# Performance work log

Measured on AMD Instinct MI355X. Metric: run time of the kernel, lower is better.

## Reference

```python
import jax, jax.numpy as jnp
import numpy as np

N_ITEMS = 100000
EMBED_DIM = 64
N_REL = 3
N_EDGES = 3200000


def setup_inputs() -> dict:
    key = jax.random.key(0)
    k1, k2, k3, k4 = jax.random.split(key, 4)
    item_embeddings = jax.random.normal(k1, (N_ITEMS, EMBED_DIM), dtype=jnp.float32)
    rows = jax.random.randint(k2, (N_REL, N_EDGES), 0, N_ITEMS, dtype=jnp.int64)
    cols = jax.random.randint(k3, (N_REL, N_EDGES), 0, N_ITEMS, dtype=jnp.int64)
    vals = jax.random.uniform(k4, (N_REL, N_EDGES), dtype=jnp.float32)
    return {"item_embeddings": item_embeddings, "rows": rows, "cols": cols, "vals": vals}


def reference(item_embeddings, rows, cols, vals):
    # item_embeddings: [N, D]; rows/cols/vals: [R, E] COO edge lists per relation.
    n_items, _ = item_embeddings.shape
    n_rel = rows.shape[0]
    rel_emb = jnp.zeros_like(item_embeddings)
    for r in range(n_rel):  # fixed small number of relation types
        # SpMM: neighbor_emb[i] = sum_{e: rows[e]==i} vals[e] * E[cols[e]]
        msgs = item_embeddings[cols[r]] * vals[r][:, None]          # [E, D]
        neighbor = jax.ops.segment_sum(msgs, rows[r], num_segments=n_items)  # [N, D]
        # degree = row sum of adjacency values, clamped to min 1
        degree = jax.ops.segment_sum(vals[r], rows[r], num_segments=n_items)  # [N]
        degree = jnp.maximum(degree, 1.0)
        rel_emb = rel_emb + neighbor / degree[:, None]
    rel_emb = rel_emb / n_rel
    return item_embeddings + rel_emb
```

## Files before the change

### kernel.cpp

```cpp
#include <hip/hip_runtime.h>

#define N_ITEMS     100000
#define EMBED_DIM   64
#define N_REL       3
#define N_EDGES     3200000
#define TOTAL_EDGES (N_REL * N_EDGES)
#define NKEY        (N_REL * N_ITEMS)

#define LOG_CH   6
#define CH_ROWS  64
#define NCHUNK   1563
#define NBKT     (NCHUNK * N_REL)
#define BCAP     2368
#define LOG_CB   12
#define NCB      25
#define TILEP    2048
#define NTILEP   ((N_EDGES + TILEP - 1) / TILEP)
#define SEGSB    68
#define CBCAP    (SEGSB * TILEP)

__global__ void initall_kernel(unsigned* __restrict__ gcursorF,
                               unsigned* __restrict__ cursorC) {
    int i = blockIdx.x * 256 + threadIdx.x;
    if (i < NBKT) gcursorF[i] = (unsigned)i * (unsigned)BCAP;
    if (i < N_REL * NCB) cursorC[i] = (unsigned)(i % NCB) * (unsigned)CBCAP;
}

__global__ void tobf16_kernel(const float* __restrict__ E, unsigned short* __restrict__ Ebf) {
    int i = blockIdx.x * 256 + threadIdx.x;
    if (i < N_ITEMS * EMBED_DIM) {
        unsigned u = __float_as_uint(E[i]);
        unsigned r = (u + 0x7FFFu + ((u >> 16) & 1u)) >> 16;
        Ebf[i] = (unsigned short)r;
    }
}

__launch_bounds__(512)
__global__ void partA2_kernel(const int* __restrict__ rows,
                              const int* __restrict__ cols,
                              const float* __restrict__ vals,
                              unsigned* __restrict__ cursorC,
                              uint2* __restrict__ coarse,
                              int rel0, unsigned relStrideU2) {
    __shared__ uint2 stag[TILEP];
    __shared__ unsigned char bkt[TILEP];
    __shared__ unsigned hist[NCB], lstart[NCB], gbase[NCB], lcur[NCB];
    int rel = rel0 + blockIdx.x / NTILEP;
    int base = (blockIdx.x % NTILEP) * TILEP;
    int cnt = N_EDGES - base; if (cnt > TILEP) cnt = TILEP;
    int t = threadIdx.x;
    const int go = rel * N_EDGES + base;
    uint2* __restrict__ coarseRel = coarse + (size_t)(rel - rel0) * relStrideU2;

    unsigned rrow[4], rcol[4], rval[4];
    #pragma unroll
    for (int k = 0; k < 4; k++) {
        int i = t + (k << 9);
        if (i < cnt) {
            rrow[k] = (unsigned)rows[go + i];
            rcol[k] = (unsigned)cols[go + i];
            rval[k] = __float_as_uint(vals[go + i]);
        } else rrow[k] = 0xFFFFFFFFu;
    }
    if (t < NCB) hist[t] = 0u;
    __syncthreads();
    #pragma unroll
    for (int k = 0; k < 4; k++)
        if (rrow[k] != 0xFFFFFFFFu) atomicAdd(&hist[rrow[k] >> LOG_CB], 1u);
    __syncthreads();
    if (t < 32) {
        unsigned v = (t < NCB) ? hist[t] : 0u;
        unsigned inc = v;
        #pragma unroll
        for (int d = 1; d < 32; d <<= 1) {
            unsigned x = __shfl_up(inc, d, 32);
            if (t >= d) inc += x;
        }
        if (t < NCB) {
            unsigned ex = inc - v;
            lstart[t] = ex; lcur[t] = ex;
            if (v) gbase[t] = atomicAdd(&cursorC[rel * NCB + t], v);
        }
    }
    __syncthreads();
    #pragma unroll
    for (int k = 0; k < 4; k++)
        if (rrow[k] != 0xFFFFFFFFu) {
            unsigned row = rrow[k];
            unsigned cb = row >> LOG_CB;
            unsigned dst = atomicAdd(&lcur[cb], 1u);
            stag[dst] = make_uint2(rcol[k] | ((row & 4095u) << 17), rval[k]);
            bkt[dst] = (unsigned char)cb;
        }
    __syncthreads();
    for (int i = t; i < cnt; i += 512) {
        unsigned bb = bkt[i];
        unsigned dst = gbase[bb] + ((unsigned)i - lstart[bb]);
        if (dst < (bb + 1u) * (unsigned)CBCAP) coarseRel[dst] = stag[i];
    }
}

__launch_bounds__(512)
__global__ void partB2_kernel(const unsigned* __restrict__ cursorC,
                              const uint2* __restrict__ coarse,
                              unsigned* __restrict__ gcursorF,
                              uint2* __restrict__ recs,
                              int rel0, unsigned relStrideU2) {
    __shared__ uint2 stag[TILEP];
    __shared__ unsigned char bkt[TILEP];
    __shared__ unsigned hist[64], lstart[64], gbase[64], lcur[64];
    int rel = rel0 + blockIdx.x / (NCB * SEGSB);
    int rem = blockIdx.x % (NCB * SEGSB);
    int cb = rem / SEGSB, seg = rem % SEGSB;
    unsigned cntA = cursorC[rel * NCB + cb] - (unsigned)cb * (unsigned)CBCAP;
    if (cntA > (unsigned)CBCAP) cntA = (unsigned)CBCAP;
    int off = seg * TILEP;
    int cnt = (int)cntA - off;
    if (cnt <= 0) return;
    if (cnt > TILEP) cnt = TILEP;
    const uint2* __restrict__ src = coarse + (size_t)(rel - rel0) * relStrideU2
                                  + (unsigned)cb * (unsigned)CBCAP + off;
    int t = threadIdx.x;

    uint2 rc[4];
    #pragma unroll
    for (int k = 0; k < 4; k++) {
        int i = t + (k << 9);
        rc[k] = (i < cnt) ? src[i] : make_uint2(0xFFFFFFFFu, 0u);
    }
    if (t < 64) hist[t] = 0u;
    __syncthreads();
    #pragma unroll
    for (int k = 0; k < 4; k++)
        if (rc[k].x != 0xFFFFFFFFu) atomicAdd(&hist[(rc[k].x >> 23) & 63u], 1u);
    __syncthreads();
    if (t < 64) {
        unsigned v = hist[t];
        unsigned inc = v;
        #pragma unroll
        for (int d = 1; d < 64; d <<= 1) {
            unsigned x = __shfl_up(inc, d, 64);
            if (t >= d) inc += x;
        }
        unsigned ex = inc - v;
        lstart[t] = ex; lcur[t] = ex;
        if (v) gbase[t] = atomicAdd(&gcursorF[(((unsigned)cb << 6) + t) * 3u + rel], v);
    }
    __syncthreads();
    #pragma unroll
    for (int k = 0; k < 4; k++)
        if (rc[k].x != 0xFFFFFFFFu) {
            unsigned j = (rc[k].x >> 23) & 63u;
            unsigned dst = atomicAdd(&lcur[j], 1u);
            stag[dst] = make_uint2(rc[k].x & 0x7FFFFFu, rc[k].y);
            bkt[dst] = (unsigned char)j;
        }
    __syncthreads();
    for (int i = t; i < cnt; i += 512) {
        unsigned j = bkt[i];
        unsigned bf = (((unsigned)cb << 6) + j) * 3u + rel;
        unsigned dst = gbase[j] + ((unsigned)i - lstart[j]);
        if (dst < (bf + 1u) * (unsigned)BCAP) recs[dst] = stag[i];
    }
}

__launch_bounds__(512, 8)
__global__ void gather_sort_kernel(const uint2* __restrict__ Ebf4,
                                   const float* __restrict__ E,
                                   const unsigned* __restrict__ gcursorF,
                                   const uint2* __restrict__ recs,
                                   float* __restrict__ out) {
    __shared__ uint2  srt[BCAP];
    __shared__ float4 accT4[CH_ROWS * 16];
    __shared__ unsigned hist[CH_ROWS], cur[CH_ROWS], rstart[CH_ROWS + 1];
    int c = blockIdx.x;
    int t = threadIdx.x;
    int w = t >> 6;
    int lane = t & 63;
    int sub = lane >> 4;
    int q = lane & 15;

    float* accT = (float*)accT4;
    for (int k = t; k < CH_ROWS * EMBED_DIM; k += 512) accT[k] = 0.f;

    for (int rel = 0; rel < N_REL; rel++) {
        unsigned b = (unsigned)(c * N_REL + rel);
        unsigned s0 = b * (unsigned)BCAP;
        int n = (int)(gcursorF[b] - s0);
        if (n > BCAP) n = BCAP;
        const uint2* __restrict__ pg = recs + s0;

        uint2 rc[5];
        #pragma unroll
        for (int k = 0; k < 5; k++) {
            int i = t + (k << 9);
            rc[k] = (i < n) ? pg[i] : make_uint2(0u, 0u);
        }
        if (t < CH_ROWS) hist[t] = 0u;
        __syncthreads();
        #pragma unroll
        for (int k = 0; k < 5; k++) {
            int i = t + (k << 9);
            if (i < n) atomicAdd(&hist[rc[k].x >> 17], 1u);
        }
        __syncthreads();
        if (t < 64) {
            unsigned v = hist[t];
            unsigned inc = v;
            #pragma unroll
            for (int d = 1; d < 64; d <<= 1) {
                unsigned x = __shfl_up(inc, d, 64);
                if (lane >= d) inc += x;
            }
            rstart[t] = inc - v;
            cur[t] = inc - v;
            if (t == 63) rstart[64] = inc;
        }
        __syncthreads();
        #pragma unroll
        for (int k = 0; k < 5; k++) {
            int i = t + (k << 9);
            if (i < n) {
                unsigned pos = atomicAdd(&cur[rc[k].x >> 17], 1u);
                srt[pos] = make_uint2(rc[k].x & 0x1FFFFu, rc[k].y);
            }
        }
        __syncthreads();

        for (int k = 0; k < 8; k++) {
            int r = (w << 3) + k;
            int base = (int)rstart[r];
            int nr = (int)(rstart[r + 1] - rstart[r]);
            float a0 = 0.f, a1 = 0.f, a2 = 0.f, a3 = 0.f, dg = 0.f;
            int i = sub;
            for (; i + 12 < nr; i += 16) {
                uint2 r0 = srt[base + i],     r1 = srt[base + i + 4];
                uint2 r2 = srt[base + i + 8], r3 = srt[base + i + 12];
                uint2 e0 = Ebf4[r0.x * 16u + q];
                uint2 e1 = Ebf4[r1.x * 16u + q];
                uint2 e2 = Ebf4[r2.x * 16u + q];
                uint2 e3 = Ebf4[r3.x * 16u + q];
                float w0 = __uint_as_float(r0.y), w1 = __uint_as_float(r1.y);
                float w2 = __uint_as_float(r2.y), w3 = __uint_as_float(r3.y);
                a0 += w0 * __uint_as_float(e0.x << 16);
                a1 += w0 * __uint_as_float(e0.x & 0xFFFF0000u);
                a2 += w0 * __uint_as_float(e0.y << 16);
                a3 += w0 * __uint_as_float(e0.y & 0xFFFF0000u);
                dg += w0;
                a0 += w1 * __uint_as_float(e1.x << 16);
                a1 += w1 * __uint_as_float(e1.x & 0xFFFF0000u);
                a2 += w1 * __uint_as_float(e1.y << 16);
                a3 += w1 * __uint_as_float(e1.y & 0xFFFF0000u);
                dg += w1;
                a0 += w2 * __uint_as_float(e2.x << 16);
                a1 += w2 * __uint_as_float(e2.x & 0xFFFF0000u);
                a2 += w2 * __uint_as_float(e2.y << 16);
                a3 += w2 * __uint_as_float(e2.y & 0xFFFF0000u);
                dg += w2;
                a0 += w3 * __uint_as_float(e3.x << 16);
                a1 += w3 * __uint_as_float(e3.x & 0xFFFF0000u);
                a2 += w3 * __uint_as_float(e3.y << 16);
                a3 += w3 * __uint_as_float(e3.y & 0xFFFF0000u);
                dg += w3;
            }
            for (; i < nr; i += 4) {
                uint2 r0 = srt[base + i];
                uint2 e0 = Ebf4[r0.x * 16u + q];
                float w0 = __uint_as_float(r0.y);
                a0 += w0 * __uint_as_float(e0.x << 16);
                a1 += w0 * __uint_as_float(e0.x & 0xFFFF0000u);
                a2 += w0 * __uint_as_float(e0.y << 16);
                a3 += w0 * __uint_as_float(e0.y & 0xFFFF0000u);
                dg += w0;
            }
            a0 += __shfl_xor(a0, 16, 64);  a0 += __shfl_xor(a0, 32, 64);
            a1 += __shfl_xor(a1, 16, 64);  a1 += __shfl_xor(a1, 32, 64);
            a2 += __shfl_xor(a2, 16, 64);  a2 += __shfl_xor(a2, 32, 64);
            a3 += __shfl_xor(a3, 16, 64);  a3 += __shfl_xor(a3, 32, 64);
            dg += __shfl_xor(dg, 16, 64);  dg += __shfl_xor(dg, 32, 64);
            float inv = 1.0f / (3.0f * fmaxf(dg, 1.0f));
            if (sub == 0) {
                float4 o = accT4[(r << 4) + q];
                accT4[(r << 4) + q] = make_float4(o.x + a0 * inv, o.y + a1 * inv,
                                                  o.z + a2 * inv, o.w + a3 * inv);
            }
        }
        __syncthreads();
    }

    int gbase2 = c * (CH_ROWS * EMBED_DIM);
    for (int k = t; k < CH_ROWS * EMBED_DIM; k += 512) {
        int gi = gbase2 + k;
        if (gi < N_ITEMS * EMBED_DIM) out[gi] = E[gi] + accT[k];
    }
}

#define NBS ((NKEY + 255) / 256)

__global__ void hist300_kernel(const int* __restrict__ rows, unsigned* __restrict__ cnt) {
    int stride = gridDim.x * blockDim.x;
    for (int i = blockIdx.x * blockDim.x + threadIdx.x; i < TOTAL_EDGES; i += stride) {
        unsigned r = (unsigned)i / (unsigned)N_EDGES;
        unsigned key = r * N_ITEMS + (unsigned)rows[i];
        atomicAdd(&cnt[key], 1u);
    }
}

__global__ void scan_blocksum(const unsigned* __restrict__ cnt, unsigned* __restrict__ bsum) {
    __shared__ unsigned s[256];
    int i = blockIdx.x * 256 + threadIdx.x;
    s[threadIdx.x] = (i < NKEY) ? cnt[i] : 0u;
    __syncthreads();
    for (int off = 128; off > 0; off >>= 1) {
        if (threadIdx.x < off) s[threadIdx.x] += s[threadIdx.x + off];
        __syncthreads();
    }
    if (threadIdx.x == 0) bsum[blockIdx.x] = s[0];
}

__global__ void scan_partials(unsigned* __restrict__ bsum, unsigned* __restrict__ starts) {
    const int IT = 5;
    int t = threadIdx.x;
    unsigned loc[IT];
    unsigned sum = 0;
    #pragma unroll
    for (int k = 0; k < IT; k++) {
        int idx = t * IT + k;
        loc[k] = (idx < NBS) ? bsum[idx] : 0u;
        sum += loc[k];
    }
    int lane = t & 63, wid = t >> 6;
    unsigned inc = sum;
    #pragma unroll
    for (int d = 1; d < 64; d <<= 1) {
        unsigned x = __shfl_up(inc, d, 64);
        if (lane >= d) inc += x;
    }
    __shared__ unsigned woff[4], woffEx[4];
    if (lane == 63) woff[wid] = inc;
    __syncthreads();
    if (t == 0) { unsigned run = 0; for (int k = 0; k < 4; k++) { woffEx[k] = run; run += woff[k]; } }
    __syncthreads();
    unsigned ex = inc - sum + woffEx[wid];
    #pragma unroll
    for (int k = 0; k < IT; k++) {
        int idx = t * IT + k;
        if (idx < NBS) { bsum[idx] = ex; ex += loc[k]; }
    }
    if (t == 0) starts[NKEY] = (unsigned)TOTAL_EDGES;
}

__global__ void scan_final(unsigned* key_arr,
                           const unsigned* __restrict__ bsum,
                           unsigned* __restrict__ cursor) {
    int i = blockIdx.x * 256 + threadIdx.x;
    unsigned v = (i < NKEY) ? key_arr[i] : 0u;
    int lane = threadIdx.x & 63, wid = threadIdx.x >> 6;
    unsigned inc = v;
    #pragma unroll
    for (int d = 1; d < 64; d <<= 1) {
        unsigned x = __shfl_up(inc, d, 64);
        if (lane >= d) inc += x;
    }
    __shared__ unsigned woff[4], woffEx[4];
    if (lane == 63) woff[wid] = inc;
    __syncthreads();
    if (threadIdx.x == 0) { unsigned run = 0; for (int k = 0; k < 4; k++) { woffEx[k] = run; run += woff[k]; } }
    __syncthreads();
    unsigned ex = inc - v + woffEx[wid] + bsum[blockIdx.x];
    if (i < NKEY) { key_arr[i] = ex; cursor[i] = ex; }
}

__global__ void binscatter2_kernel(const int* __restrict__ rows,
                                   const int* __restrict__ cols,
                                   const float* __restrict__ vals,
                                   unsigned* __restrict__ cursor,
                                   uint2* __restrict__ recs) {
    int stride = gridDim.x * blockDim.x;
    for (int i = blockIdx.x * blockDim.x + threadIdx.x; i < TOTAL_EDGES; i += stride) {
        unsigned r = (unsigned)i / (unsigned)N_EDGES;
        unsigned key = r * N_ITEMS + (unsigned)rows[i];
        unsigned pos = atomicAdd(&cursor[key], 1u);
        uint2 rec;
        rec.x = (unsigned)cols[i];
        rec.y = __float_as_uint(vals[i]);
        recs[pos] = rec;
    }
}

__launch_bounds__(192)
__global__ void gather_csr_f32_kernel(const float* __restrict__ E,
                                      const unsigned* __restrict__ starts,
                                      const uint2* __restrict__ recs,
                                      float* __restrict__ out) {
    __shared__ float part[N_REL * EMBED_DIM];
    int row = blockIdx.x;
    int w = threadIdx.x >> 6;
    int d = threadIdx.x & 63;
    unsigned key = (unsigned)w * N_ITEMS + (unsigned)row;
    unsigned s = starts[key];
    int n = (int)(starts[key + 1] - s);
    const uint2* __restrict__ p = recs + s;
    float acc = 0.0f, deg = 0.0f;
    int j = 0;
    for (; j + 8 <= n; j += 8) {
        uint2 a[8];
        #pragma unroll
        for (int k = 0; k < 8; k++) a[k] = p[j + k];
        float e[8];
        #pragma unroll
        for (int k = 0; k < 8; k++) e[k] = E[a[k].x * EMBED_DIM + d];
        #pragma unroll
        for (int k = 0; k < 8; k++) {
            float wv = __uint_as_float(a[k].y);
            acc += wv * e[k];
            deg += wv;
        }
    }
    for (; j < n; j++) {
        uint2 a = p[j];
        float wv = __uint_as_float(a.y);
        acc += wv * E[a.x * EMBED_DIM + d];
        deg += wv;
    }
    part[w * EMBED_DIM + d] = acc / (3.0f * fmaxf(deg, 1.0f));
    __syncthreads();
    if (threadIdx.x < EMBED_DIM) {
        int gi = row * EMBED_DIM + threadIdx.x;
        out[gi] = E[gi] + part[threadIdx.x]
                        + part[EMBED_DIM + threadIdx.x]
                        + part[2 * EMBED_DIM + threadIdx.x];
    }
}

__global__ void deg_kernel(const int* __restrict__ rows,
                           const float* __restrict__ vals,
                           float* __restrict__ deg) {
    long long i = (long long)blockIdx.x * blockDim.x + threadIdx.x;
    if (i >= TOTAL_EDGES) return;
    int r = (int)(i / N_EDGES);
    int row = rows[i];
    atomicAdd(&deg[(long long)r * N_ITEMS + row], vals[i]);
}

__global__ void inv_kernel(float* __restrict__ deg) {
    int i = blockIdx.x * blockDim.x + threadIdx.x;
    if (i >= N_REL * N_ITEMS) return;
    float d = deg[i];
    d = fmaxf(d, 1.0f);
    deg[i] = 1.0f / (3.0f * d);
}

__global__ void scatter_kernel(const float* __restrict__ E,
                               const int* __restrict__ rows,
                               const int* __restrict__ cols,
                               const float* __restrict__ vals,
                               const float* __restrict__ inv,
                               float* __restrict__ out) {
    long long t = (long long)blockIdx.x * blockDim.x + threadIdx.x;
    long long edge = t >> 6;
    int d = (int)(t & 63);
    if (edge >= TOTAL_EDGES) return;
    int r = (int)(edge / N_EDGES);
    int row = rows[edge];
    int col = cols[edge];
    float w = vals[edge] * inv[r * N_ITEMS + row];
    float msg = w * E[(long long)col * EMBED_DIM + d];
    atomicAdd(&out[(long long)row * EMBED_DIM + d], msg);
}

extern "C" void kernel_launch(void* const* d_in, const int* in_sizes, int n_in,
                              void* d_out, int out_size, void* d_ws, size_t ws_size,
                              hipStream_t stream) {
    const float* E    = (const float*)d_in[0];
    const int*   rows = (const int*)d_in[1];
    const int*   cols = (const int*)d_in[2];
    const float* vals = (const float*)d_in[3];
    float* out = (float*)d_out;

    const size_t GCB      = 32768;
    const size_t COARSE1  = (size_t)NCB * CBCAP * sizeof(uint2);
    const size_t FINE_B   = (size_t)NBKT * BCAP * sizeof(uint2);
    const size_t EBF_B    = (size_t)N_ITEMS * EMBED_DIM * 2;
    size_t need12 = GCB + 3 * COARSE1 + FINE_B + EBF_B;
    size_t need11 = GCB + COARSE1 + FINE_B + EBF_B;

    const size_t REGA = 1204224;
    const size_t REGC = 8192;
    const size_t RECB = (size_t)TOTAL_EDGES * sizeof(uint2);
    size_t need5 = 2 * REGA + REGC + RECB;

    if (ws_size >= need12) {
        unsigned* gcursorF = (unsigned*)d_ws;
        unsigned* cursorC  = (unsigned*)((char*)d_ws + 20480);
        uint2*    coarse   = (uint2*)((char*)d_ws + GCB);
        uint2*    recs     = (uint2*)((char*)d_ws + GCB + 3 * COARSE1);
        unsigned short* Ebf = (unsigned short*)((char*)d_ws + GCB + 3 * COARSE1 + FINE_B);

        initall_kernel<<<(NBKT + 255) / 256, 256, 0, stream>>>(gcursorF, cursorC);
        tobf16_kernel<<<(N_ITEMS * EMBED_DIM + 255) / 256, 256, 0, stream>>>(E, Ebf);
        partA2_kernel<<<N_REL * NTILEP, 512, 0, stream>>>(
            rows, cols, vals, cursorC, coarse, 0, (unsigned)(NCB * CBCAP));
        partB2_kernel<<<N_REL * NCB * SEGSB, 512, 0, stream>>>(
            cursorC, coarse, gcursorF, recs, 0, (unsigned)(NCB * CBCAP));
        gather_sort_kernel<<<NCHUNK, 512, 0, stream>>>((const uint2*)Ebf, E, gcursorF, recs, out);
    } else if (ws_size >= need11) {
        unsigned* gcursorF = (unsigned*)d_ws;
        unsigned* cursorC  = (unsigned*)((char*)d_ws + 20480);
        uint2*    coarse   = (uint2*)((char*)d_ws + GCB);
        uint2*    recs     = (uint2*)((char*)d_ws + GCB + COARSE1);
        unsigned short* Ebf = (unsigned short*)((char*)d_ws + GCB + COARSE1 + FINE_B);

        initall_kernel<<<(NBKT + 255) / 256, 256, 0, stream>>>(gcursorF, cursorC);
        tobf16_kernel<<<(N_ITEMS * EMBED_DIM + 255) / 256, 256, 0, stream>>>(E, Ebf);
        for (int r = 0; r < N_REL; r++) {
            partA2_kernel<<<NTILEP, 512, 0, stream>>>(
                rows, cols, vals, cursorC, coarse, r, 0u);
            partB2_kernel<<<NCB * SEGSB, 512, 0, stream>>>(
                cursorC, coarse, gcursorF, recs, r, 0u);
        }
        gather_sort_kernel<<<NCHUNK, 512, 0, stream>>>((const uint2*)Ebf, E, gcursorF, recs, out);
    } else if (ws_size >= need5) {
        unsigned* keyA   = (unsigned*)d_ws;
        unsigned* cursor = (unsigned*)((char*)d_ws + REGA);
        unsigned* bsum   = (unsigned*)((char*)d_ws + 2 * REGA);
        uint2*    recs   = (uint2*)((char*)d_ws + 2 * REGA + REGC);

        hipMemsetAsync(keyA, 0, NKEY * sizeof(unsigned), stream);
        hist300_kernel<<<1536, 256, 0, stream>>>(rows, keyA);
        scan_blocksum<<<NBS, 256, 0, stream>>>(keyA, bsum);
        scan_partials<<<1, 256, 0, stream>>>(bsum, keyA);
        scan_final<<<NBS, 256, 0, stream>>>(keyA, bsum, cursor);
        binscatter2_kernel<<<2048, 256, 0, stream>>>(rows, cols, vals, cursor, recs);
        gather_csr_f32_kernel<<<N_ITEMS, 192, 0, stream>>>(E, keyA, recs, out);
    } else {
        float* deg = (float*)d_ws;
        hipMemsetAsync(deg, 0, (size_t)N_REL * N_ITEMS * sizeof(float), stream);
        {
            long long total = TOTAL_EDGES;
            int block = 256;
            long long grid = (total + block - 1) / block;
            deg_kernel<<<(unsigned)grid, block, 0, stream>>>(rows, vals, deg);
        }
        {
            int total = N_REL * N_ITEMS;
            int block = 256;
            int grid = (total + block - 1) / block;
            inv_kernel<<<grid, block, 0, stream>>>(deg);
        }
        hipMemcpyAsync(out, E, (size_t)N_ITEMS * EMBED_DIM * sizeof(float),
                       hipMemcpyDeviceToDevice, stream);
        {
            long long threads = (long long)TOTAL_EDGES * 64;
            int block = 256;
            long long grid = (threads + block - 1) / block;
            scatter_kernel<<<(unsigned)grid, block, 0, stream>>>(E, rows, cols, vals, deg, out);
        }
    }
}
```

Before: 396.3 us.

## Fuse init kernels, double partition tile size, prefetch next bucket in gather

Merges the cursor-init and bf16-conversion kernels into one launch. Doubles the tile per block in both partition passes, so each thread handles 8 records and half as many blocks are launched, and adds occupancy hints to those kernels. Restructures gather_sort so the next relation's bucket is loaded into registers while the current one is sorted and gathered, hiding global load latency. The cost is more registers per thread (the launch bound drops to 4 blocks) and larger shared staging arrays.

```diff
diff --git a/kernel.cpp b/kernel.cpp
--- a/kernel.cpp
+++ b/kernel.cpp
@@ -14,20 +14,18 @@
 #define BCAP     2368
 #define LOG_CB   12
 #define NCB      25
-#define TILEP    2048
+#define TILEP    4096
 #define NTILEP   ((N_EDGES + TILEP - 1) / TILEP)
-#define SEGSB    68
+#define SEGSB    34
 #define CBCAP    (SEGSB * TILEP)
 
-__global__ void initall_kernel(unsigned* __restrict__ gcursorF,
-                               unsigned* __restrict__ cursorC) {
+__global__ void init_tobf16_kernel(const float* __restrict__ E,
+                                   unsigned short* __restrict__ Ebf,
+                                   unsigned* __restrict__ gcursorF,
+                                   unsigned* __restrict__ cursorC) {
     int i = blockIdx.x * 256 + threadIdx.x;
     if (i < NBKT) gcursorF[i] = (unsigned)i * (unsigned)BCAP;
     if (i < N_REL * NCB) cursorC[i] = (unsigned)(i % NCB) * (unsigned)CBCAP;
-}
-
-__global__ void tobf16_kernel(const float* __restrict__ E, unsigned short* __restrict__ Ebf) {
-    int i = blockIdx.x * 256 + threadIdx.x;
     if (i < N_ITEMS * EMBED_DIM) {
         unsigned u = __float_as_uint(E[i]);
         unsigned r = (u + 0x7FFFu + ((u >> 16) & 1u)) >> 16;
@@ -35,8 +33,8 @@
     }
 }
 
-__launch_bounds__(512)
-__global__ void partA2_kernel(const int* __restrict__ rows,
+__launch_bounds__(512, 8)
+__global__ void partA3_kernel(const int* __restrict__ rows,
                               const int* __restrict__ cols,
                               const float* __restrict__ vals,
                               unsigned* __restrict__ cursorC,
@@ -52,9 +50,9 @@
     const int go = rel * N_EDGES + base;
     uint2* __restrict__ coarseRel = coarse + (size_t)(rel - rel0) * relStrideU2;
 
-    unsigned rrow[4], rcol[4], rval[4];
-    #pragma unroll
-    for (int k = 0; k < 4; k++) {
+    unsigned rrow[8], rcol[8], rval[8];
+    #pragma unroll
+    for (int k = 0; k < 8; k++) {
         int i = t + (k << 9);
         if (i < cnt) {
             rrow[k] = (unsigned)rows[go + i];
@@ -65,7 +63,7 @@
     if (t < NCB) hist[t] = 0u;
     __syncthreads();
     #pragma unroll
-    for (int k = 0; k < 4; k++)
+    for (int k = 0; k < 8; k++)
         if (rrow[k] != 0xFFFFFFFFu) atomicAdd(&hist[rrow[k] >> LOG_CB], 1u);
     __syncthreads();
     if (t < 32) {
@@ -84,7 +82,7 @@
     }
     __syncthreads();
     #pragma unroll
-    for (int k = 0; k < 4; k++)
+    for (int k = 0; k < 8; k++)
         if (rrow[k] != 0xFFFFFFFFu) {
             unsigned row = rrow[k];
             unsigned cb = row >> LOG_CB;
@@ -100,8 +98,8 @@
     }
 }
 
-__launch_bounds__(512)
-__global__ void partB2_kernel(const unsigned* __restrict__ cursorC,
+__launch_bounds__(512, 8)
+__global__ void partB3_kernel(const unsigned* __restrict__ cursorC,
                               const uint2* __restrict__ coarse,
                               unsigned* __restrict__ gcursorF,
                               uint2* __restrict__ recs,
@@ -122,16 +120,16 @@
                                   + (unsigned)cb * (unsigned)CBCAP + off;
     int t = threadIdx.x;
 
-    uint2 rc[4];
-    #pragma unroll
-    for (int k = 0; k < 4; k++) {
+    uint2 rc[8];
+    #pragma unroll
+    for (int k = 0; k < 8; k++) {
         int i = t + (k << 9);
         rc[k] = (i < cnt) ? src[i] : make_uint2(0xFFFFFFFFu, 0u);
     }
     if (t < 64) hist[t] = 0u;
     __syncthreads();
     #pragma unroll
-    for (int k = 0; k < 4; k++)
+    for (int k = 0; k < 8; k++)
         if (rc[k].x != 0xFFFFFFFFu) atomicAdd(&hist[(rc[k].x >> 23) & 63u], 1u);
     __syncthreads();
     if (t < 64) {
@@ -148,7 +146,7 @@
     }
     __syncthreads();
     #pragma unroll
-    for (int k = 0; k < 4; k++)
+    for (int k = 0; k < 8; k++)
         if (rc[k].x != 0xFFFFFFFFu) {
             unsigned j = (rc[k].x >> 23) & 63u;
             unsigned dst = atomicAdd(&lcur[j], 1u);
@@ -164,7 +162,114 @@
     }
 }
 
-__launch_bounds__(512, 8)
+__device__ __forceinline__ void stage_bucket(const uint2* __restrict__ pg, int n, int t,
+                                             uint2 rc[5]) {
+    #pragma unroll
+    for (int k = 0; k < 5; k++) {
+        int i = t + (k << 9);
+        rc[k] = (i < n) ? pg[i] : make_uint2(0u, 0u);
+    }
+}
+
+__device__ __forceinline__ void sort_phase(const uint2 rc[5], int n, int t,
+                                           unsigned* hist, unsigned* cur,
+                                           unsigned* rstart, uint2* srt) {
+    if (t < CH_ROWS) hist[t] = 0u;
+    __syncthreads();
+    #pragma unroll
+    for (int k = 0; k < 5; k++) {
+        int i = t + (k << 9);
+        if (i < n) atomicAdd(&hist[rc[k].x >> 17], 1u);
+    }
+    __syncthreads();
+    if (t < 64) {
+        unsigned v = hist[t];
+        unsigned inc = v;
+        #pragma unroll
+        for (int d = 1; d < 64; d <<= 1) {
+            unsigned x = __shfl_up(inc, d, 64);
+            if (t >= d) inc += x;
+        }
+        rstart[t] = inc - v;
+        cur[t] = inc - v;
+        if (t == 63) rstart[64] = inc;
+    }
+    __syncthreads();
+    #pragma unroll
+    for (int k = 0; k < 5; k++) {
+        int i = t + (k << 9);
+        if (i < n) {
+            unsigned pos = atomicAdd(&cur[rc[k].x >> 17], 1u);
+            srt[pos] = make_uint2(rc[k].x & 0x1FFFFu, rc[k].y);
+        }
+    }
+    __syncthreads();
+}
+
+__device__ __forceinline__ void gather_phase(const uint2* __restrict__ Ebf4,
+                                             const uint2* srt, const unsigned* rstart,
+                                             float4* accT4, int w, int sub, int q) {
+    for (int k = 0; k < 8; k++) {
+        int r = (w << 3) + k;
+        int base = (int)rstart[r];
+        int nr = (int)(rstart[r + 1] - rstart[r]);
+        float a0 = 0.f, a1 = 0.f, a2 = 0.f, a3 = 0.f, dg = 0.f;
+        int i = sub;
+        for (; i + 12 < nr; i += 16) {
+            uint2 r0 = srt[base + i],     r1 = srt[base + i + 4];
+            uint2 r2 = srt[base + i + 8], r3 = srt[base + i + 12];
+            uint2 e0 = Ebf4[r0.x * 16u + q];
+            uint2 e1 = Ebf4[r1.x * 16u + q];
+            uint2 e2 = Ebf4[r2.x * 16u + q];
+            uint2 e3 = Ebf4[r3.x * 16u + q];
+            float w0 = __uint_as_float(r0.y), w1 = __uint_as_float(r1.y);
+            float w2 = __uint_as_float(r2.y), w3 = __uint_as_float(r3.y);
+            a0 += w0 * __uint_as_float(e0.x << 16);
+            a1 += w0 * __uint_as_float(e0.x & 0xFFFF0000u);
+            a2 += w0 * __uint_as_float(e0.y << 16);
+            a3 += w0 * __uint_as_float(e0.y & 0xFFFF0000u);
+            dg += w0;
+            a0 += w1 * __uint_as_float(e1.x << 16);
+            a1 += w1 * __uint_as_float(e1.x & 0xFFFF0000u);
+            a2 += w1 * __uint_as_float(e1.y << 16);
+            a3 += w1 * __uint_as_float(e1.y & 0xFFFF0000u);
+            dg += w1;
+            a0 += w2 * __uint_as_float(e2.x << 16);
+            a1 += w2 * __uint_as_float(e2.x & 0xFFFF0000u);
+            a2 += w2 * __uint_as_float(e2.y << 16);
+            a3 += w2 * __uint_as_float(e2.y & 0xFFFF0000u);
+            dg += w2;
+            a0 += w3 * __uint_as_float(e3.x << 16);
+            a1 += w3 * __uint_as_float(e3.x & 0xFFFF0000u);
+            a2 += w3 * __uint_as_float(e3.y << 16);
+            a3 += w3 * __uint_as_float(e3.y & 0xFFFF0000u);
+            dg += w3;
+        }
+        for (; i < nr; i += 4) {
+            uint2 r0 = srt[base + i];
+            uint2 e0 = Ebf4[r0.x * 16u + q];
+            float w0 = __uint_as_float(r0.y);
+            a0 += w0 * __uint_as_float(e0.x << 16);
+            a1 += w0 * __uint_as_float(e0.x & 0xFFFF0000u);
+            a2 += w0 * __uint_as_float(e0.y << 16);
+            a3 += w0 * __uint_as_float(e0.y & 0xFFFF0000u);
+            dg += w0;
+        }
+        a0 += __shfl_xor(a0, 16, 64);  a0 += __shfl_xor(a0, 32, 64);
+        a1 += __shfl_xor(a1, 16, 64);  a1 += __shfl_xor(a1, 32, 64);
+        a2 += __shfl_xor(a2, 16, 64);  a2 += __shfl_xor(a2, 32, 64);
+        a3 += __shfl_xor(a3, 16, 64);  a3 += __shfl_xor(a3, 32, 64);
+        dg += __shfl_xor(dg, 16, 64);  dg += __shfl_xor(dg, 32, 64);
+        float inv = 1.0f / (3.0f * fmaxf(dg, 1.0f));
+        if (sub == 0) {
+            float4 o = accT4[(r << 4) + q];
+            accT4[(r << 4) + q] = make_float4(o.x + a0 * inv, o.y + a1 * inv,
+                                              o.z + a2 * inv, o.w + a3 * inv);
+        }
+    }
+}
+
+__launch_bounds__(512, 4)
 __global__ void gather_sort_kernel(const uint2* __restrict__ Ebf4,
                                    const float* __restrict__ E,
                                    const unsigned* __restrict__ gcursorF,
@@ -183,110 +288,28 @@
     float* accT = (float*)accT4;
     for (int k = t; k < CH_ROWS * EMBED_DIM; k += 512) accT[k] = 0.f;
 
-    for (int rel = 0; rel < N_REL; rel++) {
-        unsigned b = (unsigned)(c * N_REL + rel);
-        unsigned s0 = b * (unsigned)BCAP;
-        int n = (int)(gcursorF[b] - s0);
-        if (n > BCAP) n = BCAP;
-        const uint2* __restrict__ pg = recs + s0;
-
-        uint2 rc[5];
-        #pragma unroll
-        for (int k = 0; k < 5; k++) {
-            int i = t + (k << 9);
-            rc[k] = (i < n) ? pg[i] : make_uint2(0u, 0u);
-        }
-        if (t < CH_ROWS) hist[t] = 0u;
-        __syncthreads();
-        #pragma unroll
-        for (int k = 0; k < 5; k++) {
-            int i = t + (k << 9);
-            if (i < n) atomicAdd(&hist[rc[k].x >> 17], 1u);
-        }
-        __syncthreads();
-        if (t < 64) {
-            unsigned v = hist[t];
-            unsigned inc = v;
-            #pragma unroll
-            for (int d = 1; d < 64; d <<= 1) {
-                unsigned x = __shfl_up(inc, d, 64);
-                if (lane >= d) inc += x;
-            }
-            rstart[t] = inc - v;
-            cur[t] = inc - v;
-            if (t == 63) rstart[64] = inc;
-        }
-        __syncthreads();
-        #pragma unroll
-        for (int k = 0; k < 5; k++) {
-            int i = t + (k << 9);
-            if (i < n) {
-                unsigned pos = atomicAdd(&cur[rc[k].x >> 17], 1u);
-                srt[pos] = make_uint2(rc[k].x & 0x1FFFFu, rc[k].y);
-            }
-        }
-        __syncthreads();
-
-        for (int k = 0; k < 8; k++) {
-            int r = (w << 3) + k;
-            int base = (int)rstart[r];
-            int nr = (int)(rstart[r + 1] - rstart[r]);
-            float a0 = 0.f, a1 = 0.f, a2 = 0.f, a3 = 0.f, dg = 0.f;
-            int i = sub;
-            for (; i + 12 < nr; i += 16) {
-                uint2 r0 = srt[base + i],     r1 = srt[base + i + 4];
-                uint2 r2 = srt[base + i + 8], r3 = srt[base + i + 12];
-                uint2 e0 = Ebf4[r0.x * 16u + q];
-                uint2 e1 = Ebf4[r1.x * 16u + q];
-                uint2 e2 = Ebf4[r2.x * 16u + q];
-                uint2 e3 = Ebf4[r3.x * 16u + q];
-                float w0 = __uint_as_float(r0.y), w1 = __uint_as_float(r1.y);
-                float w2 = __uint_as_float(r2.y), w3 = __uint_as_float(r3.y);
-                a0 += w0 * __uint_as_float(e0.x << 16);
-                a1 += w0 * __uint_as_float(e0.x & 0xFFFF0000u);
-                a2 += w0 * __uint_as_float(e0.y << 16);
-                a3 += w0 * __uint_as_float(e0.y & 0xFFFF0000u);
-                dg += w0;
-                a0 += w1 * __uint_as_float(e1.x << 16);
-                a1 += w1 * __uint_as_float(e1.x & 0xFFFF0000u);
-                a2 += w1 * __uint_as_float(e1.y << 16);
-                a3 += w1 * __uint_as_float(e1.y & 0xFFFF0000u);
-                dg += w1;
-                a0 += w2 * __uint_as_float(e2.x << 16);
-                a1 += w2 * __uint_as_float(e2.x & 0xFFFF0000u);
-                a2 += w2 * __uint_as_float(e2.y << 16);
-                a3 += w2 * __uint_as_float(e2.y & 0xFFFF0000u);
-                dg += w2;
-                a0 += w3 * __uint_as_float(e3.x << 16);
-                a1 += w3 * __uint_as_float(e3.x & 0xFFFF0000u);
-                a2 += w3 * __uint_as_float(e3.y << 16);
-                a3 += w3 * __uint_as_float(e3.y & 0xFFFF0000u);
-                dg += w3;
-            }
-            for (; i < nr; i += 4) {
-                uint2 r0 = srt[base + i];
-                uint2 e0 = Ebf4[r0.x * 16u + q];
-                float w0 = __uint_as_float(r0.y);
-                a0 += w0 * __uint_as_float(e0.x << 16);
-                a1 += w0 * __uint_as_float(e0.x & 0xFFFF0000u);
-                a2 += w0 * __uint_as_float(e0.y << 16);
-                a3 += w0 * __uint_as_float(e0.y & 0xFFFF0000u);
-                dg += w0;
-            }
-            a0 += __shfl_xor(a0, 16, 64);  a0 += __shfl_xor(a0, 32, 64);
-            a1 += __shfl_xor(a1, 16, 64);  a1 += __shfl_xor(a1, 32, 64);
-            a2 += __shfl_xor(a2, 16, 64);  a2 += __shfl_xor(a2, 32, 64);
-            a3 += __shfl_xor(a3, 16, 64);  a3 += __shfl_xor(a3, 32, 64);
-            dg += __shfl_xor(dg, 16, 64);  dg += __shfl_xor(dg, 32, 64);
-            float inv = 1.0f / (3.0f * fmaxf(dg, 1.0f));
-            if (sub == 0) {
-                float4 o = accT4[(r << 4) + q];
-                accT4[(r << 4) + q] = make_float4(o.x + a0 * inv, o.y + a1 * inv,
-                                                  o.z + a2 * inv, o.w + a3 * inv);
-            }
-        }
-        __syncthreads();
-    }
+    unsigned bBase = (unsigned)(c * N_REL);
+    int n0 = (int)(gcursorF[bBase + 0] - (bBase + 0) * (unsigned)BCAP);
+    int n1 = (int)(gcursorF[bBase + 1] - (bBase + 1) * (unsigned)BCAP);
+    int n2 = (int)(gcursorF[bBase + 2] - (bBase + 2) * (unsigned)BCAP);
+    if (n0 > BCAP) n0 = BCAP;
+    if (n1 > BCAP) n1 = BCAP;
+    if (n2 > BCAP) n2 = BCAP;
+
+    uint2 rcA[5], rcB[5];
+    stage_bucket(recs + (size_t)(bBase + 0) * BCAP, n0, t, rcA);
+
+    sort_phase(rcA, n0, t, hist, cur, rstart, srt);
+    stage_bucket(recs + (size_t)(bBase + 1) * BCAP, n1, t, rcB);
+    gather_phase(Ebf4, srt, rstart, accT4, w, sub, q);
+    __syncthreads();
+    sort_phase(rcB, n1, t, hist, cur, rstart, srt);
+    stage_bucket(recs + (size_t)(bBase + 2) * BCAP, n2, t, rcA);
+    gather_phase(Ebf4, srt, rstart, accT4, w, sub, q);
+    __syncthreads();
+    sort_phase(rcA, n2, t, hist, cur, rstart, srt);
+    gather_phase(Ebf4, srt, rstart, accT4, w, sub, q);
+    __syncthreads();
 
     int gbase2 = c * (CH_ROWS * EMBED_DIM);
     for (int k = t; k < CH_ROWS * EMBED_DIM; k += 512) {
@@ -482,7 +505,7 @@
     const size_t COARSE1  = (size_t)NCB * CBCAP * sizeof(uint2);
     const size_t FINE_B   = (size_t)NBKT * BCAP * sizeof(uint2);
     const size_t EBF_B    = (size_t)N_ITEMS * EMBED_DIM * 2;
-    size_t need12 = GCB + 3 * COARSE1 + FINE_B + EBF_B;
+    size_t need13 = GCB + 3 * COARSE1 + FINE_B + EBF_B;
     size_t need11 = GCB + COARSE1 + FINE_B + EBF_B;
 
     const size_t REGA = 1204224;
@@ -490,18 +513,19 @@
     const size_t RECB = (size_t)TOTAL_EDGES * sizeof(uint2);
     size_t need5 = 2 * REGA + REGC + RECB;
 
-    if (ws_size >= need12) {
+    int initGrid = (N_ITEMS * EMBED_DIM + 255) / 256;
+
+    if (ws_size >= need13) {
         unsigned* gcursorF = (unsigned*)d_ws;
         unsigned* cursorC  = (unsigned*)((char*)d_ws + 20480);
         uint2*    coarse   = (uint2*)((char*)d_ws + GCB);
         uint2*    recs     = (uint2*)((char*)d_ws + GCB + 3 * COARSE1);
         unsigned short* Ebf = (unsigned short*)((char*)d_ws + GCB + 3 * COARSE1 + FINE_B);
 
-        initall_kernel<<<(NBKT + 255) / 256, 256, 0, stream>>>(gcursorF, cursorC);
-        tobf16_kernel<<<(N_ITEMS * EMBED_DIM + 255) / 256, 256, 0, stream>>>(E, Ebf);
-        partA2_kernel<<<N_REL * NTILEP, 512, 0, stream>>>(
+        init_tobf16_kernel<<<initGrid, 256, 0, stream>>>(E, Ebf, gcursorF, cursorC);
+        partA3_kernel<<<N_REL * NTILEP, 512, 0, stream>>>(
             rows, cols, vals, cursorC, coarse, 0, (unsigned)(NCB * CBCAP));
-        partB2_kernel<<<N_REL * NCB * SEGSB, 512, 0, stream>>>(
+        partB3_kernel<<<N_REL * NCB * SEGSB, 512, 0, stream>>>(
             cursorC, coarse, gcursorF, recs, 0, (unsigned)(NCB * CBCAP));
         gather_sort_kernel<<<NCHUNK, 512, 0, stream>>>((const uint2*)Ebf, E, gcursorF, recs, out);
     } else if (ws_size >= need11) {
@@ -511,12 +535,11 @@
         uint2*    recs     = (uint2*)((char*)d_ws + GCB + COARSE1);
         unsigned short* Ebf = (unsigned short*)((char*)d_ws + GCB + COARSE1 + FINE_B);
 
-        initall_kernel<<<(NBKT + 255) / 256, 256, 0, stream>>>(gcursorF, cursorC);
-        tobf16_kernel<<<(N_ITEMS * EMBED_DIM + 255) / 256, 256, 0, stream>>>(E, Ebf);
+        init_tobf16_kernel<<<initGrid, 256, 0, stream>>>(E, Ebf, gcursorF, cursorC);
         for (int r = 0; r < N_REL; r++) {
-            partA2_kernel<<<NTILEP, 512, 0, stream>>>(
+            partA3_kernel<<<NTILEP, 512, 0, stream>>>(
                 rows, cols, vals, cursorC, coarse, r, 0u);
-            partB2_kernel<<<NCB * SEGSB, 512, 0, stream>>>(
+            partB3_kernel<<<NCB * SEGSB, 512, 0, stream>>>(
                 cursorC, coarse, gcursorF, recs, r, 0u);
         }
         gather_sort_kernel<<<NCHUNK, 512, 0, stream>>>((const uint2*)Ebf, E, gcursorF, recs, out);
```

Measured after the change: 405.0 us. 1.02x slower.
